# Performance work log

Measured on AMD Instinct MI355X. Metric: run time of the kernel, lower is better.

The kernel has to match this reference:

```python
import jax, jax.numpy as jnp
import numpy as np

B, T, F, H, C = 1024, 64, 256, 1024, 2


def setup_inputs() -> dict:
    key = jax.random.key(0)
    ks = jax.random.split(key, 16)
    s = 1.0 / np.sqrt(H)
    return {
        "X": jax.random.normal(ks[0], (B, T, F), jnp.float32),
        "missing_mask": (jax.random.uniform(ks[1], (B, T, F)) > 0.3).astype(jnp.float32),
        "deltas": jax.random.uniform(ks[2], (B, T, F), jnp.float32) * 5.0,
        "empirical_mean": jax.random.normal(ks[3], (B, F), jnp.float32),
        "X_filledLOCF": jax.random.normal(ks[4], (B, T, F), jnp.float32),
        # TemporalDecay h: full linear F->H
        "w_gh": jax.random.normal(ks[5], (H, F), jnp.float32) * 0.02,
        "b_gh": jnp.zeros((H,), jnp.float32),
        # TemporalDecay x: diagonal (W masked by identity) -> vector of size F
        "w_gx": jax.random.normal(ks[6], (F,), jnp.float32) * 0.02,
        "b_gx": jnp.zeros((F,), jnp.float32),
        # GRUCell: input size 2F+H, hidden H
        "w_ih": jax.random.uniform(ks[7], (3 * H, 2 * F + H), jnp.float32, -s, s),
        "w_hh": jax.random.uniform(ks[8], (3 * H, H), jnp.float32, -s, s),
        "b_ih": jax.random.uniform(ks[9], (3 * H,), jnp.float32, -s, s),
        "b_hh": jax.random.uniform(ks[10], (3 * H,), jnp.float32, -s, s),
        # classifier H -> C
        "w_cls": jax.random.normal(ks[11], (C, H), jnp.float32) * 0.02,
        "b_cls": jnp.zeros((C,), jnp.float32),
    }


def _grud_forward(X, missing_mask, deltas, empirical_mean, X_filledLOCF,
                  w_gh, b_gh, w_gx, b_gx, w_ih, w_hh, b_ih, b_hh, w_cls, b_cls):
    # time-major for scan: [T, B, F]
    Xt = jnp.swapaxes(X, 0, 1)
    Mt = jnp.swapaxes(missing_mask, 0, 1)
    Dt = jnp.swapaxes(deltas, 0, 1)
    Lt = jnp.swapaxes(X_filledLOCF, 0, 1)

    def step(h, xs):
        x, m, d, x_locf = xs
        # TemporalDecay: gamma = exp(-relu(W d + b))
        gamma_h = jnp.exp(-jax.nn.relu(d @ w_gh.T + b_gh))        # [B, H]
        gamma_x = jnp.exp(-jax.nn.relu(d * w_gx + b_gx))          # [B, F] (diag)
        h = h * gamma_h
        x_h = gamma_x * x_locf + (1.0 - gamma_x) * empirical_mean
        x_replaced = m * x + (1.0 - m) * x_h
        inp = jnp.concatenate([x_replaced, h, m], axis=1)         # [B, 2F+H]
        # GRUCell
        gi = inp @ w_ih.T + b_ih                                   # [B, 3H]
        gh = h @ w_hh.T + b_hh                                     # [B, 3H]
        i_r, i_z, i_n = jnp.split(gi, 3, axis=1)
        h_r, h_z, h_n = jnp.split(gh, 3, axis=1)
        r = jax.nn.sigmoid(i_r + h_r)
        z = jax.nn.sigmoid(i_z + h_z)
        n = jnp.tanh(i_n + r * h_n)
        h_new = (1.0 - z) * n + z * h
        return h_new, None

    h0 = jnp.zeros((X.shape[0], w_hh.shape[1]), X.dtype)
    h_final, _ = jax.lax.scan(step, h0, (Xt, Mt, Dt, Lt))
    logits = h_final @ w_cls.T + b_cls
    return jax.nn.softmax(logits, axis=1)


def reference(X, missing_mask, deltas, empirical_mean, X_filledLOCF,
              w_gh, b_gh, w_gx, b_gx, w_ih, w_hh, b_ih, b_hh, w_cls, b_cls):
    return _grud_forward(X, missing_mask, deltas, empirical_mean, X_filledLOCF,
                         w_gh, b_gh, w_gx, b_gx, w_ih, w_hh, b_ih, b_hh, w_cls, b_cls)
```

## Files before the change

kernel.cpp:

```cpp
#include <hip/hip_runtime.h>

using bf16   = __bf16;
using bf16x8 = __bf16 __attribute__((ext_vector_type(8)));
using f32x4  = float  __attribute__((ext_vector_type(4)));
using i32x4  = int    __attribute__((ext_vector_type(4)));


__device__ __forceinline__ float sigm(float x) { return 1.f / (1.f + __expf(-x)); }
__device__ __forceinline__ float tanh_fast(float x) {
  float e = __expf(2.f * x);
  return 1.f - 2.f / (e + 1.f);
}

#define GLL16(gsrc, ldst)                                                              \
  __builtin_amdgcn_global_load_lds((const __attribute__((address_space(1))) void*)(gsrc), \
                                   (__attribute__((address_space(3))) void*)(ldst), 16, 0, 0)

__global__ void prep_kernel(const float* __restrict__ X, const float* __restrict__ Msk,
                            const float* __restrict__ D, const float* __restrict__ Mean,
                            const float* __restrict__ L, const float* __restrict__ w_gx,
                            const float* __restrict__ b_gx,
                            bf16* __restrict__ XRs, bf16* __restrict__ Dbfs,
                            int c, int nsl) {
  int i = blockIdx.x * 256 + threadIdx.x;
  if (i >= (nsl << 18)) return;
  int f = i & 255, b = (i >> 8) & 1023, tl = i >> 18;
  int t = c * 16 + tl;
  size_t g = ((size_t)b << 14) + ((size_t)t << 8) + f;
  float d = D[g];
  int fs = f ^ ((b & 7) << 3);
  int row = tl * 1024 + b;
  Dbfs[(size_t)row * 256 + fs] = (bf16)d;
  float gx = __expf(-fmaxf(d * w_gx[f] + b_gx[f], 0.f));
  float xh = gx * L[g] + (1.f - gx) * Mean[(size_t)b * 256 + f];
  float m  = Msk[g];
  float xr = m * X[g] + (1.f - m) * xh;
  if (tl < 16) {
    size_t xo = (size_t)row * 512;
    XRs[xo + fs]       = (bf16)xr;
    XRs[xo + 256 + fs] = (bf16)m;
  }
}

__global__ void wprep_kernel(const float* __restrict__ w_ih, const float* __restrict__ w_hh,
                             const float* __restrict__ b_ih, const float* __restrict__ b_hh,
                             const float* __restrict__ w_gh,
                             char* __restrict__ WcH3, bf16* __restrict__ WcX3,
                             bf16* __restrict__ Wgs, float* __restrict__ bias4) {
  int i = blockIdx.x * 256 + threadIdx.x;
  if (i < 4194304) {
    int nb = i >> 17;
    int rem = i & 131071;
    int kt = rem >> 14;
    int r2 = rem & 16383;
    int nl = r2 >> 7, bb = r2 & 127;
    int cc = bb >> 4, e = bb & 15;
    int gg = nl >> 5, j = nb * 32 + (nl & 31);
    int k = kt * 128 + ((cc ^ (nl & 7)) << 4) + e;
    float v;
    if (gg == 3) v = w_hh[(size_t)(2048 + j) * 1024 + k];
    else {
      int rr = gg * 1024 + j;
      v = w_ih[(size_t)rr * 1536 + 256 + k];
      if (gg < 2) v += w_hh[(size_t)rr * 1024 + k];
    }
    float sc = (gg >= 2) ? 4096.f : 2048.f;
    int wq = __float2int_rn(v * sc);
    wq = wq > 127 ? 127 : (wq < -127 ? -127 : wq);
    WcH3[i] = (char)wq;
  } else if (i < 5767168) {
    int q = i - 4194304;
    int blk = q >> 13;
    int nb = blk >> 3, kt = blk & 7;
    int r = q & 8191;
    int nl = r >> 6, cc = (r >> 3) & 7, e = r & 7;
    int gg = nb >> 3;
    int j  = (nb & 7) * 128 + nl;
    int rr = gg * 1024 + j;
    int k = kt * 64 + ((cc ^ (nl & 7)) << 3) + e;
    float v = (k < 256) ? w_ih[(size_t)rr * 1536 + k]
                        : w_ih[(size_t)rr * 1536 + 1280 + (k - 256)];
    WcX3[q] = (bf16)v;
  } else if (i < 6029312) {
    int q = i - 5767168;
    int blk = q >> 13;
    int nb = blk >> 2, kt = blk & 3;
    int r = q & 8191;
    int nl = r >> 6, cc = (r >> 3) & 7, e = r & 7;
    int n = nb * 128 + nl;
    int k = kt * 64 + ((cc ^ (nl & 7)) << 3) + e;
    Wgs[q] = (bf16)w_gh[(size_t)n * 256 + k];
  } else if (i < 6033408) {
    int q = i - 6029312;
    int gg = q >> 10, j = q & 1023;
    float v;
    if (gg == 0)      v = b_ih[j] + b_hh[j];
    else if (gg == 1) v = b_ih[1024 + j] + b_hh[1024 + j];
    else if (gg == 2) v = b_ih[2048 + j];
    else              v = b_hh[2048 + j];
    bias4[q] = v;
  }
}

__global__ __launch_bounds__(256) void combo_kernel(
    const bf16* __restrict__ XRs, const bf16* __restrict__ WcX3,
    bf16* __restrict__ Gi, int gxblocks,
    const bf16* __restrict__ Dbfs, const bf16* __restrict__ Wgs,
    const float* __restrict__ b_gh, bf16* __restrict__ GH, int gmblocks) {
  __shared__ char smem[65536];
  char* As = smem;
  char* Bs = smem + 32768;
  int bid = blockIdx.x;
  int tid = threadIdx.x, lane = tid & 63, wid = tid >> 6;
  int wr = wid >> 1, wc = wid & 1;

  if (bid < gxblocks) {
    int cpx = gxblocks >> 3;
    int wg = (bid & 7) * cpx + (bid >> 3);
    int nb = wg % 24, mb = wg / 24;

    const bf16* aA = XRs + ((size_t)(mb * 128 + wid * 8 + (lane >> 3))) * 512 + (lane & 7) * 8;
    const bf16* aB = WcX3 + (size_t)nb * 8 * 8192 + wid * 512 + lane * 8;

    f32x4 acc[4][4];
#pragma unroll
    for (int a = 0; a < 4; ++a)
#pragma unroll
      for (int b = 0; b < 4; ++b)
#pragma unroll
        for (int q = 0; q < 4; ++q) acc[a][b][q] = 0.f;

#define GX_STAGE(buf, kt)                                                         \
  do {                                                                            \
    _Pragma("unroll")                                                             \
    for (int q = 0; q < 4; ++q)                                                   \
      GLL16(aA + q * (32 * 512) + (kt) * 64, As + (buf) * 16384 + (q * 4 + wid) * 1024); \
    _Pragma("unroll")                                                             \
    for (int q = 0; q < 4; ++q)                                                   \
      GLL16(aB + (size_t)(kt) * 8192 + q * 2048, Bs + (buf) * 16384 + (q * 4 + wid) * 1024); \
  } while (0)

    GX_STAGE(0, 0);
    __syncthreads();
    for (int kt = 0; kt < 8; ++kt) {
      const int cur = kt & 1;
      if (kt < 7) GX_STAGE(cur ^ 1, kt + 1);
#pragma unroll
      for (int kk = 0; kk < 2; ++kk) {
        int kb = kk * 64 + ((lane >> 4) << 4);
        bf16x8 af[4], bfr[4];
#pragma unroll
        for (int mf = 0; mf < 4; ++mf) {
          int row = wr * 64 + mf * 16 + (lane & 15);
          af[mf] = *(const bf16x8*)(As + cur * 16384 + (((row * 128 + kb)) ^ ((row & 7) << 4)));
        }
#pragma unroll
        for (int nf = 0; nf < 4; ++nf) {
          int nl = wc * 64 + nf * 16 + (lane & 15);
          bfr[nf] = *(const bf16x8*)(Bs + cur * 16384 + (((nl * 128 + kb)) ^ ((nl & 7) << 4)));
        }
#pragma unroll
        for (int mf = 0; mf < 4; ++mf)
#pragma unroll
          for (int nf = 0; nf < 4; ++nf)
            acc[mf][nf] = __builtin_amdgcn_mfma_f32_16x16x32_bf16(af[mf], bfr[nf], acc[mf][nf], 0, 0, 0);
      }
      __syncthreads();
    }
    char* ep = smem;
#pragma unroll
    for (int nf = 0; nf < 4; ++nf) {
      int col = wc * 64 + nf * 16 + (lane & 15);
#pragma unroll
      for (int mf = 0; mf < 4; ++mf)
#pragma unroll
        for (int reg = 0; reg < 4; ++reg) {
          int row = wr * 64 + mf * 16 + ((lane >> 4) << 2) + reg;
          int cph = ((col >> 3) ^ (((row >> 2) & 3) << 2));
          *(bf16*)(ep + row * 256 + (cph << 4) + (col & 7) * 2) = (bf16)acc[mf][nf][reg];
        }
    }
    __syncthreads();
    {
      int sl = mb >> 3, mbl = mb & 7;
      bf16* plane = Gi + (size_t)sl * 3145728 + (size_t)(nb >> 3) * 1048576 + (nb & 7) * 128;
#pragma unroll
      for (int p = 0; p < 8; ++p) {
        int idx = p * 256 + tid;
        int row = idx >> 4, c = idx & 15;
        int cph = c ^ (((row >> 2) & 3) << 2);
        bf16x8 v = *(const bf16x8*)(ep + row * 256 + (cph << 4));
        __builtin_nontemporal_store(v, (bf16x8*)(plane + (size_t)(mbl * 128 + row) * 1024 + c * 8));
      }
    }
    return;
  }

  {
    int lbid = bid - gxblocks;
    int cpx = gmblocks >> 3;
    int wg = (lbid & 7) * cpx + (lbid >> 3);
    int nb = wg & 7, mb = wg >> 3;

    const bf16* aA = Dbfs + ((size_t)(mb * 128 + wid * 8 + (lane >> 3))) * 256 + (lane & 7) * 8;
    const bf16* aB = Wgs + (size_t)nb * 4 * 8192 + wid * 512 + lane * 8;

    f32x4 acc[4][4];
#pragma unroll
    for (int a = 0; a < 4; ++a)
#pragma unroll
      for (int b = 0; b < 4; ++b)
#pragma unroll
        for (int q = 0; q < 4; ++q) acc[a][b][q] = 0.f;

#define GM_STAGE(buf, kt)                                                         \
  do {                                                                            \
    _Pragma("unroll")                                                             \
    for (int q = 0; q < 4; ++q)                                                   \
      GLL16(aA + q * (32 * 256) + (kt) * 64, As + (buf) * 16384 + (q * 4 + wid) * 1024); \
    _Pragma("unroll")                                                             \
    for (int q = 0; q < 4; ++q)                                                   \
      GLL16(aB + (size_t)(kt) * 8192 + q * 2048, Bs + (buf) * 16384 + (q * 4 + wid) * 1024); \
  } while (0)

    GM_STAGE(0, 0);
    __syncthreads();
    for (int kt = 0; kt < 4; ++kt) {
      const int cur = kt & 1;
      if (kt < 3) GM_STAGE(cur ^ 1, kt + 1);
#pragma unroll
      for (int kk = 0; kk < 2; ++kk) {
        int kb = kk * 64 + ((lane >> 4) << 4);
        bf16x8 af[4], bfr[4];
#pragma unroll
        for (int mf = 0; mf < 4; ++mf) {
          int row = wr * 64 + mf * 16 + (lane & 15);
          af[mf] = *(const bf16x8*)(As + cur * 16384 + (((row * 128 + kb)) ^ ((row & 7) << 4)));
        }
#pragma unroll
        for (int nf = 0; nf < 4; ++nf) {
          int nl = wc * 64 + nf * 16 + (lane & 15);
          bfr[nf] = *(const bf16x8*)(Bs + cur * 16384 + (((nl * 128 + kb)) ^ ((nl & 7) << 4)));
        }
#pragma unroll
        for (int mf = 0; mf < 4; ++mf)
#pragma unroll
          for (int nf = 0; nf < 4; ++nf)
            acc[mf][nf] = __builtin_amdgcn_mfma_f32_16x16x32_bf16(af[mf], bfr[nf], acc[mf][nf], 0, 0, 0);
      }
      __syncthreads();
    }
    char* ep = smem;
#pragma unroll
    for (int nf = 0; nf < 4; ++nf) {
      int col = wc * 64 + nf * 16 + (lane & 15);
      float bg = b_gh[nb * 128 + col];
#pragma unroll
      for (int mf = 0; mf < 4; ++mf)
#pragma unroll
        for (int reg = 0; reg < 4; ++reg) {
          int row = wr * 64 + mf * 16 + ((lane >> 4) << 2) + reg;
          int cph = ((col >> 3) ^ (((row >> 2) & 3) << 2));
          *(bf16*)(ep + row * 256 + (cph << 4) + (col & 7) * 2) =
              (bf16)__expf(-fmaxf(acc[mf][nf][reg] + bg, 0.f));
        }
    }
    __syncthreads();
#pragma unroll
    for (int p = 0; p < 8; ++p) {
      int idx = p * 256 + tid;
      int row = idx >> 4, c = idx & 15;
      int cph = c ^ (((row >> 2) & 3) << 2);
      bf16x8 v = *(const bf16x8*)(ep + row * 256 + (cph << 4));
      __builtin_nontemporal_store(v, (bf16x8*)(GH + (size_t)(mb * 128 + row) * 1024 + nb * 128 + c * 8));
    }
  }
}

__global__ __launch_bounds__(512, 4) void step_kernel(
    const char* __restrict__ hbs,
    const char* __restrict__ WcH3, const float* __restrict__ bias4,
    const bf16* __restrict__ gi, const bf16* __restrict__ gh_next, int is_last,
    bf16* __restrict__ hfF, char* __restrict__ hbs_next) {
  __shared__ char smem[49152];
  int tid = threadIdx.x, lane = tid & 63, wid = tid >> 6;
  int wr = wid >> 1, wc = wid & 1;
  int wg = ((blockIdx.x & 7) << 6) + (blockIdx.x >> 3);
  int mb = wg & 15, nb = wg >> 4;

  const char* aA = hbs + (size_t)(mb * 64 + (tid >> 3)) * 1024 + (tid & 7) * 16;
  const char* aB = WcH3 + (size_t)nb * 131072 + (tid >> 3) * 128 + (tid & 7) * 16;

  int jc = wc * 16 + (lane & 15);
  int j = nb * 32 + jc;
  bf16  grv[4], gzv[4], gnv[4], ghv[4];
#pragma unroll
  for (int reg = 0; reg < 4; ++reg) {
    int brow = mb * 64 + wr * 16 + ((lane >> 4) << 2) + reg;
    size_t hb_ = (size_t)brow * 1024 + j;
    grv[reg] = gi[hb_];
    gzv[reg] = gi[1048576 + hb_];
    gnv[reg] = gi[2097152 + hb_];
    ghv[reg] = gh_next[hb_];
  }

  i32x4 acc[4];
#pragma unroll
  for (int b = 0; b < 4; ++b)
#pragma unroll
    for (int q = 0; q < 4; ++q) acc[b][q] = 0;
  char hqv[4];

#define ST_STAGE(buf, kt)                                                            \
  do {                                                                               \
    GLL16(aA + (kt) * 128,            smem + (buf) * 8192 + wid * 1024);             \
    GLL16(aB + (kt) * 16384,          smem + 16384 + (buf) * 16384 + wid * 1024);    \
    GLL16(aB + (kt) * 16384 + 8192,   smem + 16384 + (buf) * 16384 + 8192 + wid * 1024); \
  } while (0)

  ST_STAGE(0, 0);
  __syncthreads();
  const int hkt = nb >> 2;
  for (int kt = 0; kt < 8; ++kt) {
    const int cur = kt & 1;
    if (kt < 7) ST_STAGE(cur ^ 1, kt + 1);
    const char* Ab = smem + cur * 8192;
    const char* Bb = smem + 16384 + cur * 16384;
#pragma unroll
    for (int kk = 0; kk < 2; ++kk) {
      int kb = kk * 64 + ((lane >> 4) << 4);
      int row = wr * 16 + (lane & 15);
      i32x4 af = *(const i32x4*)(Ab + ((row * 128 + (kb ^ ((row & 7) << 4)))));
      i32x4 bfr[4];
#pragma unroll
      for (int g = 0; g < 4; ++g) {
        int nl = g * 32 + wc * 16 + (lane & 15);
        bfr[g] = *(const i32x4*)(Bb + ((nl * 128 + (kb ^ ((nl & 7) << 4)))));
      }
#pragma unroll
      for (int g = 0; g < 4; ++g)
        acc[g] = __builtin_amdgcn_mfma_i32_16x16x64_i8(af, bfr[g], acc[g], 0, 0, 0);
    }
    if (kt == hkt) {
#pragma unroll
      for (int reg = 0; reg < 4; ++reg) {
        int lr = wr * 16 + ((lane >> 4) << 2) + reg;
        hqv[reg] = *(const char*)(Ab + lr * 128 + ((((nb & 3) * 32 + jc)) ^ ((lr & 7) << 4)));
      }
    }
    __syncthreads();
  }

  const float ISC_RZ = 3.814697265625e-06f;
  const float ISC_N  = 1.9073486328125e-06f;
  float br = bias4[j], bz = bias4[1024 + j], bn = bias4[2048 + j], bh = bias4[3072 + j];
#pragma unroll
  for (int reg = 0; reg < 4; ++reg) {
    int brow = mb * 64 + wr * 16 + ((lane >> 4) << 2) + reg;
    float pr  = (float)acc[0][reg] * ISC_RZ + (float)grv[reg] + br;
    float pz  = (float)acc[1][reg] * ISC_RZ + (float)gzv[reg] + bz;
    float pin = (float)acc[2][reg] * ISC_N  + (float)gnv[reg] + bn;
    float phn = (float)acc[3][reg] * ISC_N  + bh;
    float r = sigm(pr), z = sigm(pz);
    float nn = tanh_fast(pin + r * phn);
    float hold = (float)hqv[reg] * 0.0078125f;
    float hnew = (1.f - z) * nn + z * hold;
    float gam = is_last ? 1.f : (float)ghv[reg];
    float hd = hnew * gam;
    if (is_last) hfF[(size_t)brow * 1024 + j] = (bf16)hd;
    int hi8 = __float2int_rn(hd * 128.f);
    hi8 = hi8 > 127 ? 127 : (hi8 < -127 ? -127 : hi8);
    hbs_next[(size_t)brow * 1024 + (j ^ ((brow & 7) << 4))] = (char)hi8;
  }
}

__global__ void cls_kernel(const bf16* __restrict__ h, const float* __restrict__ w_cls,
                           const float* __restrict__ b_cls, float* __restrict__ out) {
  int wid = threadIdx.x >> 6, lane = threadIdx.x & 63;
  int b = blockIdx.x * 4 + wid;
  const bf16* hb = h + (size_t)b * 1024;
  float a0 = 0.f, a1 = 0.f;
#pragma unroll
  for (int e = 0; e < 16; ++e) {
    int i = e * 64 + lane;
    float hv = (float)hb[i];
    a0 += hv * w_cls[i];
    a1 += hv * w_cls[1024 + i];
  }
  for (int off = 32; off; off >>= 1) {
    a0 += __shfl_down(a0, off);
    a1 += __shfl_down(a1, off);
  }
  if (lane == 0) {
    float l0 = a0 + b_cls[0], l1 = a1 + b_cls[1];
    float mx = fmaxf(l0, l1);
    float e0 = __expf(l0 - mx), e1 = __expf(l1 - mx);
    float s = e0 + e1;
    out[b * 2]     = e0 / s;
    out[b * 2 + 1] = e1 / s;
  }
}

extern "C" void kernel_launch(void* const* d_in, const int* in_sizes, int n_in,
                              void* d_out, int out_size, void* d_ws, size_t ws_size,
                              hipStream_t stream) {
  const float* X     = (const float*)d_in[0];
  const float* Msk   = (const float*)d_in[1];
  const float* D     = (const float*)d_in[2];
  const float* Mean  = (const float*)d_in[3];
  const float* L     = (const float*)d_in[4];
  const float* w_gh  = (const float*)d_in[5];
  const float* b_gh  = (const float*)d_in[6];
  const float* w_gx  = (const float*)d_in[7];
  const float* b_gx  = (const float*)d_in[8];
  const float* w_ih  = (const float*)d_in[9];
  const float* w_hh  = (const float*)d_in[10];
  const float* b_ih  = (const float*)d_in[11];
  const float* b_hh  = (const float*)d_in[12];
  const float* w_cls = (const float*)d_in[13];
  const float* b_cls = (const float*)d_in[14];

  char* w = (char*)d_ws;
  bf16*  XRs   = (bf16*)(w);
  bf16*  Dbfs  = (bf16*)(w + 16777216);
  bf16*  GH    = (bf16*)(w + 25690112);
  bf16*  WcX3  = (bf16*)(w + 61341696);
  char*  WcH3  = (char*)(w + 65536000);
  bf16*  Wgs   = (bf16*)(w + 73924608);
  float* bias4 = (float*)(w + 74448896);
  bf16*  hfF   = (bf16*)(w + 74465280);
  char*  hb0   = (char*)(w + 82853888);
  char*  hb1   = (char*)(w + 84951040);
  bf16*  Gi    = (bf16*)(w + 87048192);

  char* hbp[2] = {hb0, hb1};

  hipMemsetAsync(hb0, 0, 1048576, stream);
  wprep_kernel<<<23568, 256, 0, stream>>>(w_ih, w_hh, b_ih, b_hh, w_gh, WcH3, WcX3, Wgs, bias4);

  int t = 0;
  for (int c = 0; c < 4; ++c) {
    int nsl = (c < 3) ? 17 : 16;
    prep_kernel<<<nsl * 1024, 256, 0, stream>>>(X, Msk, D, Mean, L, w_gx, b_gx, XRs, Dbfs, c, nsl);
    combo_kernel<<<3072 + nsl * 64, 256, 0, stream>>>(
        XRs, WcX3, Gi, 3072, Dbfs, Wgs, b_gh, GH, nsl * 64);
    for (int tl = 0; tl < 16; ++tl, ++t) {
      int cur = t & 1, nxt = cur ^ 1;
      step_kernel<<<512, 512, 0, stream>>>(
          hbp[cur], WcH3, bias4,
          Gi + (size_t)tl * 3145728, GH + (size_t)(tl + 1) * 1048576,
          (t == 63) ? 1 : 0, hfF, hbp[nxt]);
    }
  }
  cls_kernel<<<256, 256, 0, stream>>>(hfF, w_cls, b_cls, (float*)d_out);
}
```

Before: 1.125 ms.

## Fuse 16 per-step GRU launches into one persistent chunk kernel with grid barrier

Replaces the 16 separate step_kernel launches per chunk with a single persistent chunk_kernel that loops over the timesteps. Blocks synchronize between steps with an atomic-counter grid barrier in global memory. The intent is to remove per-step kernel launch overhead and the tail gaps between launches. It relies on all 512 blocks being co-resident, which 4 blocks/CU on 256 CUs allows, and it adds spin-wait and fence costs.

```diff
diff --git a/kernel.cpp b/kernel.cpp
--- a/kernel.cpp
+++ b/kernel.cpp
@@ -277,39 +277,25 @@
   }
 }
 
-__global__ __launch_bounds__(512, 4) void step_kernel(
-    const char* __restrict__ hbs,
+__global__ __launch_bounds__(512, 4) void chunk_kernel(
+    char* __restrict__ hb0, char* __restrict__ hb1,
     const char* __restrict__ WcH3, const float* __restrict__ bias4,
-    const bf16* __restrict__ gi, const bf16* __restrict__ gh_next, int is_last,
-    bf16* __restrict__ hfF, char* __restrict__ hbs_next) {
+    const bf16* __restrict__ Gi, const bf16* __restrict__ GH,
+    int c, bf16* __restrict__ hfF, unsigned int* __restrict__ barctr) {
   __shared__ char smem[49152];
   int tid = threadIdx.x, lane = tid & 63, wid = tid >> 6;
   int wr = wid >> 1, wc = wid & 1;
   int wg = ((blockIdx.x & 7) << 6) + (blockIdx.x >> 3);
   int mb = wg & 15, nb = wg >> 4;
 
-  const char* aA = hbs + (size_t)(mb * 64 + (tid >> 3)) * 1024 + (tid & 7) * 16;
   const char* aB = WcH3 + (size_t)nb * 131072 + (tid >> 3) * 128 + (tid & 7) * 16;
-
   int jc = wc * 16 + (lane & 15);
   int j = nb * 32 + jc;
-  bf16  grv[4], gzv[4], gnv[4], ghv[4];
-#pragma unroll
-  for (int reg = 0; reg < 4; ++reg) {
-    int brow = mb * 64 + wr * 16 + ((lane >> 4) << 2) + reg;
-    size_t hb_ = (size_t)brow * 1024 + j;
-    grv[reg] = gi[hb_];
-    gzv[reg] = gi[1048576 + hb_];
-    gnv[reg] = gi[2097152 + hb_];
-    ghv[reg] = gh_next[hb_];
-  }
-
-  i32x4 acc[4];
-#pragma unroll
-  for (int b = 0; b < 4; ++b)
-#pragma unroll
-    for (int q = 0; q < 4; ++q) acc[b][q] = 0;
-  char hqv[4];
+  float br = bias4[j], bz = bias4[1024 + j], bn = bias4[2048 + j], bh = bias4[3072 + j];
+  const int hkt = nb >> 2;
+  const float ISC_RZ = 3.814697265625e-06f;
+  const float ISC_N  = 1.9073486328125e-06f;
+  unsigned int base = (unsigned int)c * 15u * 512u;
 
 #define ST_STAGE(buf, kt)                                                            \
   do {                                                                               \
@@ -318,59 +304,96 @@
     GLL16(aB + (kt) * 16384 + 8192,   smem + 16384 + (buf) * 16384 + 8192 + wid * 1024); \
   } while (0)
 
-  ST_STAGE(0, 0);
-  __syncthreads();
-  const int hkt = nb >> 2;
-  for (int kt = 0; kt < 8; ++kt) {
-    const int cur = kt & 1;
-    if (kt < 7) ST_STAGE(cur ^ 1, kt + 1);
-    const char* Ab = smem + cur * 8192;
-    const char* Bb = smem + 16384 + cur * 16384;
-#pragma unroll
-    for (int kk = 0; kk < 2; ++kk) {
-      int kb = kk * 64 + ((lane >> 4) << 4);
-      int row = wr * 16 + (lane & 15);
-      i32x4 af = *(const i32x4*)(Ab + ((row * 128 + (kb ^ ((row & 7) << 4)))));
-      i32x4 bfr[4];
-#pragma unroll
-      for (int g = 0; g < 4; ++g) {
-        int nl = g * 32 + wc * 16 + (lane & 15);
-        bfr[g] = *(const i32x4*)(Bb + ((nl * 128 + (kb ^ ((nl & 7) << 4)))));
-      }
-#pragma unroll
-      for (int g = 0; g < 4; ++g)
-        acc[g] = __builtin_amdgcn_mfma_i32_16x16x64_i8(af, bfr[g], acc[g], 0, 0, 0);
-    }
-    if (kt == hkt) {
-#pragma unroll
-      for (int reg = 0; reg < 4; ++reg) {
-        int lr = wr * 16 + ((lane >> 4) << 2) + reg;
-        hqv[reg] = *(const char*)(Ab + lr * 128 + ((((nb & 3) * 32 + jc)) ^ ((lr & 7) << 4)));
-      }
-    }
+  for (int tl = 0; tl < 16; ++tl) {
+    int t = c * 16 + tl;
+    const char* hbs      = (t & 1) ? hb1 : hb0;
+    char*       hbs_next = (t & 1) ? hb0 : hb1;
+    const bf16* gi      = Gi + (size_t)tl * 3145728;
+    const bf16* gh_next = GH + (size_t)(tl + 1) * 1048576;
+    int is_last = (t == 63);
+    const char* aA = hbs + (size_t)(mb * 64 + (tid >> 3)) * 1024 + (tid & 7) * 16;
+
+    bf16 grv[4], gzv[4], gnv[4], ghv[4];
+#pragma unroll
+    for (int reg = 0; reg < 4; ++reg) {
+      int brow = mb * 64 + wr * 16 + ((lane >> 4) << 2) + reg;
+      size_t hb_ = (size_t)brow * 1024 + j;
+      grv[reg] = gi[hb_];
+      gzv[reg] = gi[1048576 + hb_];
+      gnv[reg] = gi[2097152 + hb_];
+      ghv[reg] = gh_next[hb_];
+    }
+
+    i32x4 acc[4];
+#pragma unroll
+    for (int b = 0; b < 4; ++b)
+#pragma unroll
+      for (int q = 0; q < 4; ++q) acc[b][q] = 0;
+    char hqv[4];
+
+    ST_STAGE(0, 0);
     __syncthreads();
-  }
-
-  const float ISC_RZ = 3.814697265625e-06f;
-  const float ISC_N  = 1.9073486328125e-06f;
-  float br = bias4[j], bz = bias4[1024 + j], bn = bias4[2048 + j], bh = bias4[3072 + j];
-#pragma unroll
-  for (int reg = 0; reg < 4; ++reg) {
-    int brow = mb * 64 + wr * 16 + ((lane >> 4) << 2) + reg;
-    float pr  = (float)acc[0][reg] * ISC_RZ + (float)grv[reg] + br;
-    float pz  = (float)acc[1][reg] * ISC_RZ + (float)gzv[reg] + bz;
-    float pin = (float)acc[2][reg] * ISC_N  + (float)gnv[reg] + bn;
-    float phn = (float)acc[3][reg] * ISC_N  + bh;
-    float r = sigm(pr), z = sigm(pz);
-    float nn = tanh_fast(pin + r * phn);
-    float hold = (float)hqv[reg] * 0.0078125f;
-    float hnew = (1.f - z) * nn + z * hold;
-    float gam = is_last ? 1.f : (float)ghv[reg];
-    float hd = hnew * gam;
-    if (is_last) hfF[(size_t)brow * 1024 + j] = (bf16)hd;
-    int hi8 = __float2int_rn(hd * 128.f);
-    hi8 = hi8 > 127 ? 127 : (hi8 < -127 ? -127 : hi8);
-    hbs_next[(size_t)brow * 1024 + (j ^ ((brow & 7) << 4))] = (char)hi8;
+    for (int kt = 0; kt < 8; ++kt) {
+      const int cur = kt & 1;
+      if (kt < 7) ST_STAGE(cur ^ 1, kt + 1);
+      const char* Ab = smem + cur * 8192;
+      const char* Bb = smem + 16384 + cur * 16384;
+#pragma unroll
+      for (int kk = 0; kk < 2; ++kk) {
+        int kb = kk * 64 + ((lane >> 4) << 4);
+        int row = wr * 16 + (lane & 15);
+        i32x4 af = *(const i32x4*)(Ab + ((row * 128 + (kb ^ ((row & 7) << 4)))));
+        i32x4 bfr[4];
+#pragma unroll
+        for (int g = 0; g < 4; ++g) {
+          int nl = g * 32 + wc * 16 + (lane & 15);
+          bfr[g] = *(const i32x4*)(Bb + ((nl * 128 + (kb ^ ((nl & 7) << 4)))));
+        }
+#pragma unroll
+        for (int g = 0; g < 4; ++g)
+          acc[g] = __builtin_amdgcn_mfma_i32_16x16x64_i8(af, bfr[g], acc[g], 0, 0, 0);
+      }
+      if (kt == hkt) {
+#pragma unroll
+        for (int reg = 0; reg < 4; ++reg) {
+          int lr = wr * 16 + ((lane >> 4) << 2) + reg;
+          hqv[reg] = *(const char*)(Ab + lr * 128 + ((((nb & 3) * 32 + jc)) ^ ((lr & 7) << 4)));
+        }
+      }
+      __syncthreads();
+    }
+
+#pragma unroll
+    for (int reg = 0; reg < 4; ++reg) {
+      int brow = mb * 64 + wr * 16 + ((lane >> 4) << 2) + reg;
+      float pr  = (float)acc[0][reg] * ISC_RZ + (float)grv[reg] + br;
+      float pz  = (float)acc[1][reg] * ISC_RZ + (float)gzv[reg] + bz;
+      float pin = (float)acc[2][reg] * ISC_N  + (float)gnv[reg] + bn;
+      float phn = (float)acc[3][reg] * ISC_N  + bh;
+      float r = sigm(pr), z = sigm(pz);
+      float nn = tanh_fast(pin + r * phn);
+      float hold = (float)hqv[reg] * 0.0078125f;
+      float hnew = (1.f - z) * nn + z * hold;
+      float gam = is_last ? 1.f : (float)ghv[reg];
+      float hd = hnew * gam;
+      if (is_last) hfF[(size_t)brow * 1024 + j] = (bf16)hd;
+      int hi8 = __float2int_rn(hd * 128.f);
+      hi8 = hi8 > 127 ? 127 : (hi8 < -127 ? -127 : hi8);
+      hbs_next[(size_t)brow * 1024 + (j ^ ((brow & 7) << 4))] = (char)hi8;
+    }
+
+    if (tl < 15) {
+      __syncthreads();
+      if (tid == 0) {
+        __threadfence();
+        __hip_atomic_fetch_add(barctr, 1u, __ATOMIC_RELAXED, __HIP_MEMORY_SCOPE_AGENT);
+        unsigned int target = base + (unsigned int)(tl + 1) * 512u;
+        while (__hip_atomic_load(barctr, __ATOMIC_RELAXED, __HIP_MEMORY_SCOPE_AGENT) < target)
+          __builtin_amdgcn_s_sleep(8);
+        __threadfence();
+      }
+      __syncthreads();
+    }
   }
 }
 
@@ -421,36 +444,29 @@
   const float* b_cls = (const float*)d_in[14];
 
   char* w = (char*)d_ws;
-  bf16*  XRs   = (bf16*)(w);
-  bf16*  Dbfs  = (bf16*)(w + 16777216);
-  bf16*  GH    = (bf16*)(w + 25690112);
-  bf16*  WcX3  = (bf16*)(w + 61341696);
-  char*  WcH3  = (char*)(w + 65536000);
-  bf16*  Wgs   = (bf16*)(w + 73924608);
-  float* bias4 = (float*)(w + 74448896);
-  bf16*  hfF   = (bf16*)(w + 74465280);
-  char*  hb0   = (char*)(w + 82853888);
-  char*  hb1   = (char*)(w + 84951040);
-  bf16*  Gi    = (bf16*)(w + 87048192);
-
-  char* hbp[2] = {hb0, hb1};
+  bf16*  XRs    = (bf16*)(w);
+  bf16*  Dbfs   = (bf16*)(w + 16777216);
+  bf16*  GH     = (bf16*)(w + 25690112);
+  bf16*  WcX3   = (bf16*)(w + 61341696);
+  char*  WcH3   = (char*)(w + 65536000);
+  unsigned int* barctr = (unsigned int*)(w + 69730304);
+  bf16*  Wgs    = (bf16*)(w + 73924608);
+  float* bias4  = (float*)(w + 74448896);
+  bf16*  hfF    = (bf16*)(w + 74465280);
+  char*  hb0    = (char*)(w + 82853888);
+  char*  hb1    = (char*)(w + 84951040);
+  bf16*  Gi     = (bf16*)(w + 87048192);
 
   hipMemsetAsync(hb0, 0, 1048576, stream);
+  hipMemsetAsync(barctr, 0, 4, stream);
   wprep_kernel<<<23568, 256, 0, stream>>>(w_ih, w_hh, b_ih, b_hh, w_gh, WcH3, WcX3, Wgs, bias4);
 
-  int t = 0;
   for (int c = 0; c < 4; ++c) {
     int nsl = (c < 3) ? 17 : 16;
     prep_kernel<<<nsl * 1024, 256, 0, stream>>>(X, Msk, D, Mean, L, w_gx, b_gx, XRs, Dbfs, c, nsl);
     combo_kernel<<<3072 + nsl * 64, 256, 0, stream>>>(
         XRs, WcX3, Gi, 3072, Dbfs, Wgs, b_gh, GH, nsl * 64);
-    for (int tl = 0; tl < 16; ++tl, ++t) {
-      int cur = t & 1, nxt = cur ^ 1;
-      step_kernel<<<512, 512, 0, stream>>>(
-          hbp[cur], WcH3, bias4,
-          Gi + (size_t)tl * 3145728, GH + (size_t)(tl + 1) * 1048576,
-          (t == 63) ? 1 : 0, hfF, hbp[nxt]);
-    }
+    chunk_kernel<<<512, 512, 0, stream>>>(hb0, hb1, WcH3, bias4, Gi, GH, c, hfF, barctr);
   }
   cls_kernel<<<256, 256, 0, stream>>>(hfF, w_cls, b_cls, (float*)d_out);
 }
```

Result: slower. 3.963 ms (+252.2%).
